# Kernel tuning notes

Hardware: AMD Instinct MI355X
Metric: run time of the kernel (lower is better)

The kernel has to match this reference:

```python
import jax, jax.numpy as jnp
import numpy as np

N_NODES = 50000
N_EDGES = 800000
D_IN = 128
D_OUT = 128
BN_EPS = 1e-5

# (component index, sign) per (column block j, row block i) of the octonion
# Hamilton matrix, matching make_octonion_mul's cat order exactly.
_OCT_TABLE = [
    [(0, 1), (1, -1), (2, -1), (3, -1), (4, -1), (5, -1), (6, -1), (7, -1)],
    [(1, 1), (0, 1), (3, -1), (2, 1), (5, -1), (4, 1), (7, 1), (6, -1)],
    [(2, 1), (3, 1), (0, 1), (1, -1), (6, -1), (7, -1), (4, 1), (5, 1)],
    [(3, 1), (2, -1), (1, 1), (0, 1), (7, -1), (6, 1), (5, -1), (4, 1)],
    [(4, 1), (5, 1), (6, 1), (7, 1), (0, 1), (1, -1), (2, -1), (3, -1)],
    [(5, 1), (4, -1), (7, 1), (6, -1), (1, 1), (0, 1), (3, 1), (2, -1)],
    [(6, 1), (7, -1), (4, -1), (5, 1), (2, 1), (3, -1), (0, 1), (1, 1)],
    [(7, 1), (6, 1), (5, -1), (4, -1), (3, 1), (2, 1), (1, -1), (0, 1)],
]


def make_octonion_mul(kernel):
    # kernel: [D_IN//8, D_OUT] -> hamilton: [D_IN, D_OUT]
    e = jnp.split(kernel, 8, axis=1)
    cols = [jnp.concatenate([s * e[i] for (i, s) in col], axis=0)
            for col in _OCT_TABLE]
    return jnp.concatenate(cols, axis=1)


def setup_inputs() -> dict:
    key = jax.random.key(0)
    k1, k2, k3, k4, k5 = jax.random.split(key, 5)
    stdv = np.sqrt(6.0 / (D_IN // 8 + D_OUT))
    return {
        "input": jax.random.normal(k1, (N_NODES, D_IN), dtype=jnp.float32),
        "adj_row": jax.random.randint(k2, (N_EDGES,), 0, N_NODES, dtype=jnp.int32),
        "adj_col": jax.random.randint(k3, (N_EDGES,), 0, N_NODES, dtype=jnp.int32),
        "adj_val": jax.random.uniform(k4, (N_EDGES,), dtype=jnp.float32),
        "weight": jax.random.uniform(k5, (D_IN // 8, D_OUT), dtype=jnp.float32,
                                     minval=-stdv, maxval=stdv),
        "gamma": jnp.ones((D_OUT,), dtype=jnp.float32),
        "beta": jnp.zeros((D_OUT,), dtype=jnp.float32),
    }


def reference(input, adj_row, adj_col, adj_val, weight, gamma, beta):
    hamilton = make_octonion_mul(weight)             # [D_IN, D_OUT]
    support = input @ hamilton                       # [N, D_OUT]
    # sparse adjacency spmm: out[r] += val * support[c]
    msg = adj_val[:, None] * support[adj_col]        # [E, D_OUT]
    out = jax.ops.segment_sum(msg, adj_row, num_segments=N_NODES)
    # BatchNorm1d (training mode: biased batch stats), then tanh
    mean = jnp.mean(out, axis=0)
    var = jnp.var(out, axis=0)
    normed = (out - mean) / jnp.sqrt(var + BN_EPS) * gamma + beta
    return jnp.tanh(normed)
```

## Files before the change

kernel.cpp:

```cpp
#include <hip/hip_runtime.h>
#include <hip/hip_fp16.h>
#include <math.h>

#define N_NODES 50000
#define N_EDGES 800000
#define D 128
#define BN_EPS 1e-5f
#define N_TILES 3125
#define CAP 64
#define SPMM_BLOCKS 2048
#define SCOLS 32
#define BINS 512
#define RPB 98
#define EPB 3125
#define SORTB 256
#define BCAP 2048
#define GEMMB 782

typedef __attribute__((ext_vector_type(8))) _Float16 half8;
typedef __attribute__((ext_vector_type(4))) float floatx4;

__device__ __constant__ int OCT_C[8][8] = {
    {0,1,2,3,4,5,6,7},
    {1,0,3,2,5,4,7,6},
    {2,3,0,1,6,7,4,5},
    {3,2,1,0,7,6,5,4},
    {4,5,6,7,0,1,2,3},
    {5,4,7,6,1,0,3,2},
    {6,7,4,5,2,3,0,1},
    {7,6,5,4,3,2,1,0}};
__device__ __constant__ float OCT_S[8][8] = {
    { 1,-1,-1,-1,-1,-1,-1,-1},
    { 1, 1,-1, 1,-1, 1, 1,-1},
    { 1, 1, 1,-1,-1,-1, 1, 1},
    { 1,-1, 1, 1,-1, 1,-1, 1},
    { 1, 1, 1, 1, 1,-1,-1,-1},
    { 1,-1, 1,-1, 1, 1, 1,-1},
    { 1,-1,-1, 1, 1,-1, 1, 1},
    { 1, 1,-1,-1, 1, 1,-1, 1}};

__global__ __launch_bounds__(256) void setup_kernel(const float* __restrict__ W,
                                                    __half* __restrict__ Ht,
                                                    float* __restrict__ stats,
                                                    int* __restrict__ bintail) {
    const int i = blockIdx.x * 256 + threadIdx.x;
    if (i < D * D) {
        int ccol = i >> 7, k = i & 127;
        int ii = k >> 4, kw = k & 15, j = ccol >> 4, m = ccol & 15;
        Ht[i] = __float2half(OCT_S[j][ii] * W[kw * D + OCT_C[j][ii] * 16 + m]);
    }
    if (i < 2 * D) stats[i] = 0.0f;
    if (i < BINS * 16) bintail[i] = 0;
}

__global__ __launch_bounds__(256) void sortgemm_kernel(const int* __restrict__ arow,
                                                       const int* __restrict__ acol,
                                                       const float* __restrict__ aval,
                                                       int* __restrict__ bintail,
                                                       uint2* __restrict__ binned,
                                                       const float* __restrict__ in,
                                                       const __half* __restrict__ Ht,
                                                       __half* __restrict__ support) {
    __shared__ int hist[BINS], lbase[BINS], hist2[BINS];
    const int b = blockIdx.x;
    const int tid = threadIdx.x;
    if (b < SORTB) {
        for (int k = tid; k < BINS; k += 256) hist[k] = 0;
        __syncthreads();
        const int e0 = b * EPB, e1 = e0 + EPB;
        for (int i = e0 + tid; i < e1; i += 256) {
            int bin = arow[i] / RPB;
            atomicAdd(&hist[bin], 1);
        }
        __syncthreads();
        for (int k = tid; k < BINS; k += 256) {
            lbase[k] = atomicAdd(&bintail[k * 16], hist[k]);
            hist2[k] = 0;
        }
        __syncthreads();
        for (int i = e0 + tid; i < e1; i += 256) {
            int r = arow[i];
            int bin = r / RPB;
            unsigned hv = (unsigned)__half_as_ushort(__float2half(aval[i]));
            unsigned pk = ((unsigned)acol[i] & 0xFFFFu) | (hv << 16);
            int k = atomicAdd(&hist2[bin], 1);
            int idx = lbase[bin] + k;
            if (idx < BCAP) binned[(size_t)bin * BCAP + idx] = make_uint2(pk, (unsigned)r);
        }
        return;
    }
    const int wv = tid >> 6;
    const int tile = (b - SORTB) * 4 + wv;
    if (tile >= N_TILES) return;
    const int lane = tid & 63;
    const int s = lane & 15;
    const int t = lane >> 4;

    half8 bb[8][4];
#pragma unroll
    for (int kk = 0; kk < 4; ++kk)
#pragma unroll
        for (int n = 0; n < 8; ++n)
            bb[n][kk] = *reinterpret_cast<const half8*>(Ht + (size_t)(16 * n + s) * D + kk * 32 + 8 * t);

    const float* ap = in + (size_t)(tile * 16 + s) * D;
    half8 a[4];
#pragma unroll
    for (int kk = 0; kk < 4; ++kk) {
        float4 f0 = *reinterpret_cast<const float4*>(ap + kk * 32 + 8 * t);
        float4 f1 = *reinterpret_cast<const float4*>(ap + kk * 32 + 8 * t + 4);
        a[kk][0] = (_Float16)f0.x; a[kk][1] = (_Float16)f0.y;
        a[kk][2] = (_Float16)f0.z; a[kk][3] = (_Float16)f0.w;
        a[kk][4] = (_Float16)f1.x; a[kk][5] = (_Float16)f1.y;
        a[kk][6] = (_Float16)f1.z; a[kk][7] = (_Float16)f1.w;
    }

    floatx4 acc[8];
#pragma unroll
    for (int n = 0; n < 8; ++n) acc[n] = (floatx4){0.f, 0.f, 0.f, 0.f};
#pragma unroll
    for (int kk = 0; kk < 4; ++kk)
#pragma unroll
        for (int n = 0; n < 8; ++n)
            acc[n] = __builtin_amdgcn_mfma_f32_16x16x32_f16(a[kk], bb[n][kk], acc[n], 0, 0, 0);

    __half* sp = support + (size_t)(tile * 16 + 4 * t) * D + s;
#pragma unroll
    for (int r = 0; r < 4; ++r)
#pragma unroll
        for (int n = 0; n < 8; ++n)
            sp[(size_t)r * D + 16 * n] = __float2half(acc[n][r]);
}

__global__ __launch_bounds__(256) void bucket_kernel(const int* __restrict__ bintail,
                                                     const uint2* __restrict__ binned,
                                                     int* __restrict__ cnt,
                                                     unsigned* __restrict__ bucket) {
    __shared__ int lcnt[RPB];
    const int b = blockIdx.x;
    const int tid = threadIdx.x;
    if (tid < RPB) lcnt[tid] = 0;
    __syncthreads();
    const int nb = bintail[b * 16];
    const uint2* seg = binned + (size_t)b * BCAP;
    const int rbase = b * RPB;
    for (int i = tid; i < nb; i += 256) {
        uint2 e = seg[i];
        int rl = (int)e.y - rbase;
        int slot = atomicAdd(&lcnt[rl], 1);
        if (slot < CAP) bucket[(size_t)(rbase + rl) * CAP + slot] = e.x;
    }
    __syncthreads();
    if (tid < RPB && rbase + tid < N_NODES) cnt[rbase + tid] = lcnt[tid];
}

__global__ __launch_bounds__(256) void spmm_kernel(const __half* __restrict__ support,
                                                   const int* __restrict__ cnt,
                                                   const unsigned* __restrict__ bucket,
                                                   __half* __restrict__ outh,
                                                   float* __restrict__ colsum,
                                                   float* __restrict__ colsq) {
    const int tid = threadIdx.x;
    const int lane = tid & 63;
    const int wv = tid >> 6;
    const int h = lane >> 4;
    const int cl = lane & 15;
    const int b = blockIdx.x;
    const int slice = (b & 7) >> 1;
    const int rank = ((b >> 3) << 1) | (b & 1);
    const int nrank = SPMM_BLOCKS >> 2;
    const int colbase = slice * SCOLS + cl * 2;
    const unsigned cb2 = (unsigned)(colbase * 2);
    const char* sbase = reinterpret_cast<const char*>(support);

    __shared__ float lsum[SCOLS], lsq[SCOLS];
    if (tid < SCOLS) { lsum[tid] = 0.f; lsq[tid] = 0.f; }
    __syncthreads();

    float s0 = 0.f, s1 = 0.f, q0 = 0.f, q1 = 0.f;

    for (int row = rank * 8 + wv * 2; row < N_NODES; row += nrank * 8) {
        const int rowb = row + 1;
        int na = cnt[row]; na = na < CAP ? na : CAP;
        int nb = (rowb < N_NODES) ? cnt[rowb] : 0; nb = nb < CAP ? nb : CAP;
        const unsigned ewa = (lane < na) ? bucket[(size_t)row * CAP + lane] : 0u;
        const unsigned ewb = (lane < nb) ? bucket[(size_t)rowb * CAP + lane] : 0u;
        __half2 acca = __half2half2(__ushort_as_half((unsigned short)0));
        __half2 accb = acca;
        const int nmax = na > nb ? na : nb;
        const int n16 = (nmax + 15) & ~15;
        for (int e = 0; e < n16; e += 16) {
            unsigned ua[4], ub[4];
            __half2 ga[4], gb[4];
#pragma unroll
            for (int j = 0; j < 4; ++j) {
                int idx = e + j * 4 + h;
                ua[j] = __shfl(ewa, idx);
                ub[j] = __shfl(ewb, idx);
            }
#pragma unroll
            for (int j = 0; j < 4; ++j) {
                unsigned offa = ((ua[j] & 0xFFFFu) << 8) + cb2;
                unsigned offb = ((ub[j] & 0xFFFFu) << 8) + cb2;
                ga[j] = *reinterpret_cast<const __half2*>(sbase + offa);
                gb[j] = *reinterpret_cast<const __half2*>(sbase + offb);
            }
#pragma unroll
            for (int j = 0; j < 4; ++j) {
                unsigned va2 = __builtin_amdgcn_perm(ua[j], ua[j], 0x07060706u);
                unsigned vb2 = __builtin_amdgcn_perm(ub[j], ub[j], 0x07060706u);
                acca = __hfma2(*reinterpret_cast<__half2*>(&va2), ga[j], acca);
                accb = __hfma2(*reinterpret_cast<__half2*>(&vb2), gb[j], accb);
            }
        }
#pragma unroll
        for (int off = 16; off <= 32; off <<= 1) {
            int ia = __shfl_xor(*reinterpret_cast<int*>(&acca), off);
            int ib = __shfl_xor(*reinterpret_cast<int*>(&accb), off);
            acca = __hadd2(acca, *reinterpret_cast<__half2*>(&ia));
            accb = __hadd2(accb, *reinterpret_cast<__half2*>(&ib));
        }
        if (h == 0) {
            float2 fa = __half22float2(acca);
            *reinterpret_cast<__half2*>(outh + (size_t)row * D + colbase) = acca;
            s0 += fa.x; s1 += fa.y; q0 += fa.x * fa.x; q1 += fa.y * fa.y;
            if (rowb < N_NODES) {
                float2 fb = __half22float2(accb);
                *reinterpret_cast<__half2*>(outh + (size_t)rowb * D + colbase) = accb;
                s0 += fb.x; s1 += fb.y; q0 += fb.x * fb.x; q1 += fb.y * fb.y;
            }
        }
    }

    if (h == 0) {
        atomicAdd(&lsum[cl * 2 + 0], s0); atomicAdd(&lsum[cl * 2 + 1], s1);
        atomicAdd(&lsq[cl * 2 + 0], q0);  atomicAdd(&lsq[cl * 2 + 1], q1);
    }
    __syncthreads();
    if (tid < SCOLS) {
        atomicAdd(&colsum[slice * SCOLS + tid], lsum[tid]);
        atomicAdd(&colsq[slice * SCOLS + tid], lsq[tid]);
    }
}

__global__ __launch_bounds__(256) void bn_tanh_kernel(const __half* __restrict__ outh,
                                                      float* __restrict__ out,
                                                      const float* __restrict__ colsum,
                                                      const float* __restrict__ colsq,
                                                      const float* __restrict__ gamma,
                                                      const float* __restrict__ beta) {
    __shared__ float scale[D], shift[D];
    const int tid = threadIdx.x;
    if (tid < D) {
        float mean = colsum[tid] * (1.0f / N_NODES);
        float var  = colsq[tid] * (1.0f / N_NODES) - mean * mean;
        float sc   = rsqrtf(var + BN_EPS) * gamma[tid];
        scale[tid] = sc;
        shift[tid] = beta[tid] - mean * sc;
    }
    __syncthreads();
    const int nq = N_NODES * D / 8;
    floatx4* outv = reinterpret_cast<floatx4*>(out);
    for (int i = blockIdx.x * 256 + tid; i < nq; i += gridDim.x * 256) {
        uint4 v = reinterpret_cast<const uint4*>(outh)[i];
        const int c = (i & 15) * 8;
        float r[8];
        float2 f;
        f = __half22float2(*reinterpret_cast<__half2*>(&v.x)); r[0] = f.x; r[1] = f.y;
        f = __half22float2(*reinterpret_cast<__half2*>(&v.y)); r[2] = f.x; r[3] = f.y;
        f = __half22float2(*reinterpret_cast<__half2*>(&v.z)); r[4] = f.x; r[5] = f.y;
        f = __half22float2(*reinterpret_cast<__half2*>(&v.w)); r[6] = f.x; r[7] = f.y;
#pragma unroll
        for (int k = 0; k < 8; ++k) {
            float x = r[k] * scale[c + k] + shift[c + k];
            float e = __expf(2.0f * x);
            r[k] = 1.0f - 2.0f / (1.0f + e);
        }
        floatx4 o0 = {r[0], r[1], r[2], r[3]};
        floatx4 o1 = {r[4], r[5], r[6], r[7]};
        __builtin_nontemporal_store(o0, outv + i * 2 + 0);
        __builtin_nontemporal_store(o1, outv + i * 2 + 1);
    }
}

extern "C" void kernel_launch(void* const* d_in, const int* in_sizes, int n_in,
                              void* d_out, int out_size, void* d_ws, size_t ws_size,
                              hipStream_t stream) {
    const float* input  = (const float*)d_in[0];
    const int*   arow   = (const int*)d_in[1];
    const int*   acol   = (const int*)d_in[2];
    const float* aval   = (const float*)d_in[3];
    const float* weight = (const float*)d_in[4];
    const float* gamma  = (const float*)d_in[5];
    const float* beta   = (const float*)d_in[6];
    float* out = (float*)d_out;

    __half*   support = (__half*)d_ws;
    unsigned* bucket  = (unsigned*)(support + (size_t)N_NODES * D);
    __half*   outh    = (__half*)(bucket + (size_t)N_NODES * CAP);
    uint2*    binned  = (uint2*)outh;
    int*      cnt     = (int*)(outh + (size_t)N_NODES * D);
    float*    colsum  = (float*)(cnt + N_NODES);
    int*      bintail = (int*)(colsum + 2 * D);
    __half*   Ht      = (__half*)(bintail + BINS * 16);

    setup_kernel<<<64, 256, 0, stream>>>(weight, Ht, colsum, bintail);
    sortgemm_kernel<<<SORTB + GEMMB, 256, 0, stream>>>(arow, acol, aval, bintail, binned,
                                                       input, Ht, support);
    bucket_kernel<<<BINS, 256, 0, stream>>>(bintail, binned, cnt, bucket);
    spmm_kernel<<<SPMM_BLOCKS, 256, 0, stream>>>(support, cnt, bucket, outh, colsum, colsum + D);
    bn_tanh_kernel<<<2048, 256, 0, stream>>>(outh, out, colsum, colsum + D, gamma, beta);
}
```

Before: 102.9 us.

## Fuse bucket build into SpMM using per-block shared-memory row buckets

Removes the separate bucket kernel and its global bucket/cnt arrays. Each SpMM block rebuilds the CSR-like buckets for its own bin of 98 rows in shared memory from the binned edge list, then processes those rows, reading edge indices from LDS instead of a global buffer plus shuffles. This saves a launch and a global write/read of the bucket array. In exchange, the four column-slice blocks that share a bin each redo the bucketing, and the 25KB of LDS per block may lower occupancy. Rows are now assigned contiguously per block instead of strided.

```diff
diff --git a/kernel.cpp b/kernel.cpp
--- a/kernel.cpp
+++ b/kernel.cpp
@@ -132,62 +132,54 @@
             sp[(size_t)r * D + 16 * n] = __float2half(acc[n][r]);
 }
 
-__global__ __launch_bounds__(256) void bucket_kernel(const int* __restrict__ bintail,
-                                                     const uint2* __restrict__ binned,
-                                                     int* __restrict__ cnt,
-                                                     unsigned* __restrict__ bucket) {
+__global__ __launch_bounds__(256) void spmm_kernel(const int* __restrict__ bintail,
+                                                   const uint2* __restrict__ binned,
+                                                   const __half* __restrict__ support,
+                                                   __half* __restrict__ outh,
+                                                   float* __restrict__ colsum,
+                                                   float* __restrict__ colsq) {
+    __shared__ unsigned lbucket[RPB * CAP];
     __shared__ int lcnt[RPB];
+    __shared__ float lsum[SCOLS], lsq[SCOLS];
+
+    const int tid = threadIdx.x;
     const int b = blockIdx.x;
-    const int tid = threadIdx.x;
+    const int slice = (b & 7) >> 1;
+    const int rank = ((b >> 3) << 1) | (b & 1);
+    const int rbase = rank * RPB;
+
     if (tid < RPB) lcnt[tid] = 0;
+    if (tid < SCOLS) { lsum[tid] = 0.f; lsq[tid] = 0.f; }
     __syncthreads();
-    const int nb = bintail[b * 16];
-    const uint2* seg = binned + (size_t)b * BCAP;
-    const int rbase = b * RPB;
+    int nb = bintail[rank * 16];
+    nb = nb < BCAP ? nb : BCAP;
+    const uint2* seg = binned + (size_t)rank * BCAP;
     for (int i = tid; i < nb; i += 256) {
         uint2 e = seg[i];
         int rl = (int)e.y - rbase;
         int slot = atomicAdd(&lcnt[rl], 1);
-        if (slot < CAP) bucket[(size_t)(rbase + rl) * CAP + slot] = e.x;
+        if (slot < CAP) lbucket[rl * CAP + slot] = e.x;
     }
     __syncthreads();
-    if (tid < RPB && rbase + tid < N_NODES) cnt[rbase + tid] = lcnt[tid];
-}
-
-__global__ __launch_bounds__(256) void spmm_kernel(const __half* __restrict__ support,
-                                                   const int* __restrict__ cnt,
-                                                   const unsigned* __restrict__ bucket,
-                                                   __half* __restrict__ outh,
-                                                   float* __restrict__ colsum,
-                                                   float* __restrict__ colsq) {
-    const int tid = threadIdx.x;
+
     const int lane = tid & 63;
     const int wv = tid >> 6;
     const int h = lane >> 4;
     const int cl = lane & 15;
-    const int b = blockIdx.x;
-    const int slice = (b & 7) >> 1;
-    const int rank = ((b >> 3) << 1) | (b & 1);
-    const int nrank = SPMM_BLOCKS >> 2;
     const int colbase = slice * SCOLS + cl * 2;
     const unsigned cb2 = (unsigned)(colbase * 2);
     const char* sbase = reinterpret_cast<const char*>(support);
 
-    __shared__ float lsum[SCOLS], lsq[SCOLS];
-    if (tid < SCOLS) { lsum[tid] = 0.f; lsq[tid] = 0.f; }
-    __syncthreads();
-
     float s0 = 0.f, s1 = 0.f, q0 = 0.f, q1 = 0.f;
 
-    for (int row = rank * 8 + wv * 2; row < N_NODES; row += nrank * 8) {
+    for (int rl = wv * 2; rl < RPB; rl += 8) {
+        const int row = rbase + rl;
         const int rowb = row + 1;
-        int na = cnt[row]; na = na < CAP ? na : CAP;
-        int nb = (rowb < N_NODES) ? cnt[rowb] : 0; nb = nb < CAP ? nb : CAP;
-        const unsigned ewa = (lane < na) ? bucket[(size_t)row * CAP + lane] : 0u;
-        const unsigned ewb = (lane < nb) ? bucket[(size_t)rowb * CAP + lane] : 0u;
+        int na = lcnt[rl]; na = na < CAP ? na : CAP;
+        int nb2 = (rl + 1 < RPB) ? lcnt[rl + 1] : 0; nb2 = nb2 < CAP ? nb2 : CAP;
         __half2 acca = __half2half2(__ushort_as_half((unsigned short)0));
         __half2 accb = acca;
-        const int nmax = na > nb ? na : nb;
+        const int nmax = na > nb2 ? na : nb2;
         const int n16 = (nmax + 15) & ~15;
         for (int e = 0; e < n16; e += 16) {
             unsigned ua[4], ub[4];
@@ -195,8 +187,8 @@
 #pragma unroll
             for (int j = 0; j < 4; ++j) {
                 int idx = e + j * 4 + h;
-                ua[j] = __shfl(ewa, idx);
-                ub[j] = __shfl(ewb, idx);
+                ua[j] = (idx < na)  ? lbucket[rl * CAP + idx] : 0u;
+                ub[j] = (idx < nb2) ? lbucket[(rl + 1) * CAP + idx] : 0u;
             }
 #pragma unroll
             for (int j = 0; j < 4; ++j) {
@@ -221,10 +213,12 @@
             accb = __hadd2(accb, *reinterpret_cast<__half2*>(&ib));
         }
         if (h == 0) {
-            float2 fa = __half22float2(acca);
-            *reinterpret_cast<__half2*>(outh + (size_t)row * D + colbase) = acca;
-            s0 += fa.x; s1 += fa.y; q0 += fa.x * fa.x; q1 += fa.y * fa.y;
-            if (rowb < N_NODES) {
+            if (row < N_NODES) {
+                float2 fa = __half22float2(acca);
+                *reinterpret_cast<__half2*>(outh + (size_t)row * D + colbase) = acca;
+                s0 += fa.x; s1 += fa.y; q0 += fa.x * fa.x; q1 += fa.y * fa.y;
+            }
+            if (rowb < N_NODES && rl + 1 < RPB) {
                 float2 fb = __half22float2(accb);
                 *reinterpret_cast<__half2*>(outh + (size_t)rowb * D + colbase) = accb;
                 s0 += fb.x; s1 += fb.y; q0 += fb.x * fb.x; q1 += fb.y * fb.y;
@@ -296,18 +290,17 @@
     float* out = (float*)d_out;
 
     __half*   support = (__half*)d_ws;
-    unsigned* bucket  = (unsigned*)(support + (size_t)N_NODES * D);
-    __half*   outh    = (__half*)(bucket + (size_t)N_NODES * CAP);
-    uint2*    binned  = (uint2*)outh;
-    int*      cnt     = (int*)(outh + (size_t)N_NODES * D);
-    float*    colsum  = (float*)(cnt + N_NODES);
+    __half*   outh    = (__half*)(support + (size_t)N_NODES * D);
+    uint2*    binned  = (uint2*)(outh + (size_t)N_NODES * D);
+    float*    colsum  = (float*)(binned + (size_t)BINS * BCAP);
+    float*    colsq   = colsum + D;
     int*      bintail = (int*)(colsum + 2 * D);
     __half*   Ht      = (__half*)(bintail + BINS * 16);
 
     setup_kernel<<<64, 256, 0, stream>>>(weight, Ht, colsum, bintail);
     sortgemm_kernel<<<SORTB + GEMMB, 256, 0, stream>>>(arow, acol, aval, bintail, binned,
                                                        input, Ht, support);
-    bucket_kernel<<<BINS, 256, 0, stream>>>(bintail, binned, cnt, bucket);
-    spmm_kernel<<<SPMM_BLOCKS, 256, 0, stream>>>(support, cnt, bucket, outh, colsum, colsum + D);
-    bn_tanh_kernel<<<2048, 256, 0, stream>>>(outh, out, colsum, colsum + D, gamma, beta);
-}
+    spmm_kernel<<<SPMM_BLOCKS, 256, 0, stream>>>(bintail, binned, support, outh,
+                                                 colsum, colsq);
+    bn_tanh_kernel<<<2048, 256, 0, stream>>>(outh, out, colsum, colsq, gamma, beta);
+}
```

Measured after the change: 99.12 us. 1.04x faster.
